# Kernel tuning notes

Hardware: AMD Instinct MI355X
Metric: run time of the kernel (lower is better)

## Reference

```python
import jax, jax.numpy as jnp
import numpy as np

HARD_DIST_CUTOFF = 2.0  # init kwarg of ExternalNeighbors


def setup_inputs() -> dict:
    key = jax.random.key(0)
    ks = jax.random.split(key, 6)
    n_mol, n_atoms = 128, 1024
    n_real = n_mol * n_atoms          # 131072
    n_pairs = 8388608                 # ~64 neighbors per atom
    coordinates = jax.random.normal(ks[0], (n_mol, n_atoms, 3), dtype=jnp.float32)
    real_atoms = jax.random.randint(ks[1], (n_real,), 0, n_mol * n_atoms, dtype=jnp.int64)
    shifts = jax.random.randint(ks[2], (n_pairs, 3), 0, 2, dtype=jnp.int32)
    cell = jax.random.normal(ks[3], (3, 3), dtype=jnp.float32)
    pair_first = jax.random.randint(ks[4], (n_pairs,), 0, n_real, dtype=jnp.int64)
    pair_second = jax.random.randint(ks[5], (n_pairs,), 0, n_real, dtype=jnp.int64)
    return {"coordinates": coordinates, "real_atoms": real_atoms, "shifts": shifts,
            "cell": cell, "pair_first": pair_first, "pair_second": pair_second}


def reference(coordinates, real_atoms, shifts, cell, pair_first, pair_second):
    n_mol, n_atoms, _ = coordinates.shape
    # gather real-atom coordinates from flattened (mol*atom, 3)
    atom_coordinates = coordinates.reshape(n_mol * n_atoms, 3)[real_atoms]
    # pair displacement with periodic shift: [n_pairs, 3]
    paircoord = (atom_coordinates[pair_second] - atom_coordinates[pair_first]
                 + shifts.astype(cell.dtype) @ cell)
    distflat = jnp.linalg.norm(paircoord, axis=1)  # [n_pairs]
    # torch version does boolean compaction (dynamic shape); in jax we keep
    # fixed shape and zero/mask-out pairs beyond the cutoff, returning the mask.
    mask = distflat < HARD_DIST_CUTOFF
    distflat_m = jnp.where(mask, distflat, 0.0)
    pair_first_m = jnp.where(mask, pair_first, -1)
    pair_second_m = jnp.where(mask, pair_second, -1)
    paircoord_m = jnp.where(mask[:, None], paircoord, 0.0)
    return distflat_m, pair_first_m, pair_second_m, paircoord_m, mask
```

## Files before the change

### kernel.cpp

```cpp
#include <hip/hip_runtime.h>


typedef float f32x4 __attribute__((ext_vector_type(4)));
typedef int   i32x4 __attribute__((ext_vector_type(4)));

#define HARD_DIST_CUTOFF 2.0f

__global__ __launch_bounds__(256) void build_gather_table(
    const float* __restrict__ coords,
    const int*   __restrict__ real_atoms,
    f32x4* __restrict__ tab,
    int n_real)
{
    const int i = blockIdx.x * blockDim.x + threadIdx.x;
    if (i < n_real) {
        const int a = __builtin_nontemporal_load(real_atoms + i);
        const float* c = coords + 3 * (size_t)a;
        f32x4 v;
        v.x = c[0]; v.y = c[1]; v.z = c[2]; v.w = 0.0f;
        tab[i] = v;
    }
}

__global__ __launch_bounds__(256, 8) void external_neighbors_v4(
    const f32x4* __restrict__ tab,
    const int*   __restrict__ shifts,
    const float* __restrict__ cell,
    const int*   __restrict__ pair_first,
    const int*   __restrict__ pair_second,
    float* __restrict__ out,
    int n_pairs)
{
    const float c00 = cell[0], c01 = cell[1], c02 = cell[2];
    const float c10 = cell[3], c11 = cell[4], c12 = cell[5];
    const float c20 = cell[6], c21 = cell[7], c22 = cell[8];

    const size_t N = (size_t)n_pairs;
    float* __restrict__ out_dist = out;
    float* __restrict__ out_pf   = out + N;
    float* __restrict__ out_ps   = out + 2 * N;
    float* __restrict__ out_pc   = out + 3 * N;
    float* __restrict__ out_mask = out + 6 * N;

    const int tid    = blockIdx.x * blockDim.x + threadIdx.x;
    const int nthr   = gridDim.x * blockDim.x;
    const int nbatch = n_pairs >> 2;

    for (int b = tid; b < nbatch; b += nthr) {
        const int base = b << 2;

        const i32x4 pf4 = __builtin_nontemporal_load(
            reinterpret_cast<const i32x4*>(pair_first + base));
        const i32x4 ps4 = __builtin_nontemporal_load(
            reinterpret_cast<const i32x4*>(pair_second + base));
        const i32x4* sh = reinterpret_cast<const i32x4*>(shifts + 3 * (size_t)base);
        const i32x4 sA = __builtin_nontemporal_load(sh + 0);
        const i32x4 sB = __builtin_nontemporal_load(sh + 1);
        const i32x4 sC = __builtin_nontemporal_load(sh + 2);

        const int pf[4] = {pf4.x, pf4.y, pf4.z, pf4.w};
        const int ps[4] = {ps4.x, ps4.y, ps4.z, ps4.w};
        const int s0[4] = {sA.x, sA.w, sB.z, sC.y};
        const int s1[4] = {sA.y, sB.x, sB.w, sC.z};
        const int s2[4] = {sA.z, sB.y, sC.x, sC.w};

        f32x4 A[4], B[4];
        #pragma unroll
        for (int k = 0; k < 4; ++k) A[k] = tab[pf[k]];
        #pragma unroll
        for (int k = 0; k < 4; ++k) B[k] = tab[ps[k]];

        f32x4 dist, pfo, pso, msk;
        float dxv[4], dyv[4], dzv[4];
        #pragma unroll
        for (int k = 0; k < 4; ++k) {
            const float f0 = (float)s0[k], f1 = (float)s1[k], f2 = (float)s2[k];
            const float dx = B[k].x - A[k].x + f0 * c00 + f1 * c10 + f2 * c20;
            const float dy = B[k].y - A[k].y + f0 * c01 + f1 * c11 + f2 * c21;
            const float dz = B[k].z - A[k].z + f0 * c02 + f1 * c12 + f2 * c22;
            const float d  = sqrtf(dx * dx + dy * dy + dz * dz);
            const bool  m  = d < HARD_DIST_CUTOFF;
            dist[k] = m ? d : 0.0f;
            pfo[k]  = m ? (float)pf[k] : -1.0f;
            pso[k]  = m ? (float)ps[k] : -1.0f;
            msk[k]  = m ? 1.0f : 0.0f;
            dxv[k]  = m ? dx : 0.0f;
            dyv[k]  = m ? dy : 0.0f;
            dzv[k]  = m ? dz : 0.0f;
        }

        __builtin_nontemporal_store(dist, reinterpret_cast<f32x4*>(out_dist + base));
        __builtin_nontemporal_store(pfo,  reinterpret_cast<f32x4*>(out_pf   + base));
        __builtin_nontemporal_store(pso,  reinterpret_cast<f32x4*>(out_ps   + base));
        __builtin_nontemporal_store(msk,  reinterpret_cast<f32x4*>(out_mask + base));
        f32x4* pc = reinterpret_cast<f32x4*>(out_pc + 3 * (size_t)base);
        const f32x4 p0 = {dxv[0], dyv[0], dzv[0], dxv[1]};
        const f32x4 p1 = {dyv[1], dzv[1], dxv[2], dyv[2]};
        const f32x4 p2 = {dzv[2], dxv[3], dyv[3], dzv[3]};
        __builtin_nontemporal_store(p0, pc + 0);
        __builtin_nontemporal_store(p1, pc + 1);
        __builtin_nontemporal_store(p2, pc + 2);
    }

    for (int p = (nbatch << 2) + tid; p < n_pairs; p += nthr) {
        const int pfs = pair_first[p];
        const int pss = pair_second[p];
        const float f0 = (float)shifts[3 * p + 0];
        const float f1 = (float)shifts[3 * p + 1];
        const float f2 = (float)shifts[3 * p + 2];
        const f32x4 Aa = tab[pfs];
        const f32x4 Bb = tab[pss];
        const float dx = Bb.x - Aa.x + f0 * c00 + f1 * c10 + f2 * c20;
        const float dy = Bb.y - Aa.y + f0 * c01 + f1 * c11 + f2 * c21;
        const float dz = Bb.z - Aa.z + f0 * c02 + f1 * c12 + f2 * c22;
        const float d  = sqrtf(dx * dx + dy * dy + dz * dz);
        const bool  m  = d < HARD_DIST_CUTOFF;
        out_dist[p] = m ? d : 0.0f;
        out_pf[p]   = m ? (float)pfs : -1.0f;
        out_ps[p]   = m ? (float)pss : -1.0f;
        out_pc[3*(size_t)p+0] = m ? dx : 0.0f;
        out_pc[3*(size_t)p+1] = m ? dy : 0.0f;
        out_pc[3*(size_t)p+2] = m ? dz : 0.0f;
        out_mask[p] = m ? 1.0f : 0.0f;
    }
}

__global__ __launch_bounds__(256) void external_neighbors_v2(
    const float* __restrict__ coords,
    const int*   __restrict__ real_atoms,
    const int*   __restrict__ shifts,
    const float* __restrict__ cell,
    const int*   __restrict__ pair_first,
    const int*   __restrict__ pair_second,
    float* __restrict__ out,
    int n_pairs)
{
    const float c00 = cell[0], c01 = cell[1], c02 = cell[2];
    const float c10 = cell[3], c11 = cell[4], c12 = cell[5];
    const float c20 = cell[6], c21 = cell[7], c22 = cell[8];
    const size_t N = (size_t)n_pairs;
    float* out_dist = out;
    float* out_pf   = out + N;
    float* out_ps   = out + 2 * N;
    float* out_pc   = out + 3 * N;
    float* out_mask = out + 6 * N;
    const int tid = blockIdx.x * blockDim.x + threadIdx.x;
    const int stride = gridDim.x * blockDim.x;
    for (int p = tid; p < n_pairs; p += stride) {
        const int pfs = pair_first[p];
        const int pss = pair_second[p];
        const float f0 = (float)shifts[3 * p + 0];
        const float f1 = (float)shifts[3 * p + 1];
        const float f2 = (float)shifts[3 * p + 2];
        const int iaa = real_atoms[pfs];
        const int ibb = real_atoms[pss];
        const float dx = coords[3*ibb+0] - coords[3*iaa+0] + f0*c00 + f1*c10 + f2*c20;
        const float dy = coords[3*ibb+1] - coords[3*iaa+1] + f0*c01 + f1*c11 + f2*c21;
        const float dz = coords[3*ibb+2] - coords[3*iaa+2] + f0*c02 + f1*c12 + f2*c22;
        const float d  = sqrtf(dx*dx + dy*dy + dz*dz);
        const bool  m  = d < HARD_DIST_CUTOFF;
        out_dist[p] = m ? d : 0.0f;
        out_pf[p]   = m ? (float)pfs : -1.0f;
        out_ps[p]   = m ? (float)pss : -1.0f;
        out_pc[3*(size_t)p+0] = m ? dx : 0.0f;
        out_pc[3*(size_t)p+1] = m ? dy : 0.0f;
        out_pc[3*(size_t)p+2] = m ? dz : 0.0f;
        out_mask[p] = m ? 1.0f : 0.0f;
    }
}

extern "C" void kernel_launch(void* const* d_in, const int* in_sizes, int n_in,
                              void* d_out, int out_size, void* d_ws, size_t ws_size,
                              hipStream_t stream) {
    const float* coords      = (const float*)d_in[0];
    const int*   real_atoms  = (const int*)d_in[1];
    const int*   shifts      = (const int*)d_in[2];
    const float* cell        = (const float*)d_in[3];
    const int*   pair_first  = (const int*)d_in[4];
    const int*   pair_second = (const int*)d_in[5];
    float*       out         = (float*)d_out;

    const int n_real  = in_sizes[1];
    const int n_pairs = in_sizes[4];

    const size_t tab_bytes = (size_t)n_real * sizeof(f32x4);

    if (ws_size >= tab_bytes) {
        f32x4* tab = (f32x4*)d_ws;
        build_gather_table<<<(n_real + 255) / 256, 256, 0, stream>>>(
            coords, real_atoms, tab, n_real);

        external_neighbors_v4<<<2048, 256, 0, stream>>>(
            tab, shifts, cell, pair_first, pair_second, out, n_pairs);
    } else {
        external_neighbors_v2<<<2048, 256, 0, stream>>>(
            coords, real_atoms, shifts, cell, pair_first, pair_second, out, n_pairs);
    }
}
```

Measured before the change: 442.8 us.

## Stage paircoord writes through LDS and launch one 4-pair batch per thread

Replaces the grid-stride loop with a non-persistent grid where each thread handles exactly four pairs, sized as n_pairs/1024 blocks. The interleaved paircoord output is transposed through LDS so each wave writes contiguous 16-byte chunks across lanes, aiming for fully coalesced stores instead of per-thread 48-byte strided writes. Input loads drop the nontemporal hint and the occupancy launch bound is removed. The fast path now requires n_pairs divisible by 1024 and adds a block-wide barrier plus 12 KB of LDS per block.

After: 404.8 us. 1.09x faster.

```diff
diff --git a/kernel.cpp b/kernel.cpp
--- a/kernel.cpp
+++ b/kernel.cpp
@@ -14,7 +14,7 @@
 {
     const int i = blockIdx.x * blockDim.x + threadIdx.x;
     if (i < n_real) {
-        const int a = __builtin_nontemporal_load(real_atoms + i);
+        const int a = real_atoms[i];
         const float* c = coords + 3 * (size_t)a;
         f32x4 v;
         v.x = c[0]; v.y = c[1]; v.z = c[2]; v.w = 0.0f;
@@ -22,7 +22,7 @@
     }
 }
 
-__global__ __launch_bounds__(256, 8) void external_neighbors_v4(
+__global__ __launch_bounds__(256) void external_neighbors_v6(
     const f32x4* __restrict__ tab,
     const int*   __restrict__ shifts,
     const float* __restrict__ cell,
@@ -31,6 +31,8 @@
     float* __restrict__ out,
     int n_pairs)
 {
+    __shared__ float lds_pc[4][768];
+
     const float c00 = cell[0], c01 = cell[1], c02 = cell[2];
     const float c10 = cell[3], c11 = cell[4], c12 = cell[5];
     const float c20 = cell[6], c21 = cell[7], c22 = cell[8];
@@ -42,86 +44,63 @@
     float* __restrict__ out_pc   = out + 3 * N;
     float* __restrict__ out_mask = out + 6 * N;
 
-    const int tid    = blockIdx.x * blockDim.x + threadIdx.x;
-    const int nthr   = gridDim.x * blockDim.x;
-    const int nbatch = n_pairs >> 2;
+    const int tid  = blockIdx.x * blockDim.x + threadIdx.x;
+    const int base = tid << 2;
+    const int wv   = threadIdx.x >> 6;
+    const int lane = threadIdx.x & 63;
 
-    for (int b = tid; b < nbatch; b += nthr) {
-        const int base = b << 2;
+    const i32x4 pf4 = *reinterpret_cast<const i32x4*>(pair_first  + base);
+    const i32x4 ps4 = *reinterpret_cast<const i32x4*>(pair_second + base);
+    const i32x4* sh = reinterpret_cast<const i32x4*>(shifts + 3 * (size_t)base);
+    const i32x4 sA = sh[0], sB = sh[1], sC = sh[2];
 
-        const i32x4 pf4 = __builtin_nontemporal_load(
-            reinterpret_cast<const i32x4*>(pair_first + base));
-        const i32x4 ps4 = __builtin_nontemporal_load(
-            reinterpret_cast<const i32x4*>(pair_second + base));
-        const i32x4* sh = reinterpret_cast<const i32x4*>(shifts + 3 * (size_t)base);
-        const i32x4 sA = __builtin_nontemporal_load(sh + 0);
-        const i32x4 sB = __builtin_nontemporal_load(sh + 1);
-        const i32x4 sC = __builtin_nontemporal_load(sh + 2);
+    const int pf[4] = {pf4.x, pf4.y, pf4.z, pf4.w};
+    const int ps[4] = {ps4.x, ps4.y, ps4.z, ps4.w};
+    const int s0[4] = {sA.x, sA.w, sB.z, sC.y};
+    const int s1[4] = {sA.y, sB.x, sB.w, sC.z};
+    const int s2[4] = {sA.z, sB.y, sC.x, sC.w};
 
-        const int pf[4] = {pf4.x, pf4.y, pf4.z, pf4.w};
-        const int ps[4] = {ps4.x, ps4.y, ps4.z, ps4.w};
-        const int s0[4] = {sA.x, sA.w, sB.z, sC.y};
-        const int s1[4] = {sA.y, sB.x, sB.w, sC.z};
-        const int s2[4] = {sA.z, sB.y, sC.x, sC.w};
+    f32x4 A[4], B[4];
+    #pragma unroll
+    for (int k = 0; k < 4; ++k) A[k] = tab[pf[k]];
+    #pragma unroll
+    for (int k = 0; k < 4; ++k) B[k] = tab[ps[k]];
 
-        f32x4 A[4], B[4];
-        #pragma unroll
-        for (int k = 0; k < 4; ++k) A[k] = tab[pf[k]];
-        #pragma unroll
-        for (int k = 0; k < 4; ++k) B[k] = tab[ps[k]];
-
-        f32x4 dist, pfo, pso, msk;
-        float dxv[4], dyv[4], dzv[4];
-        #pragma unroll
-        for (int k = 0; k < 4; ++k) {
-            const float f0 = (float)s0[k], f1 = (float)s1[k], f2 = (float)s2[k];
-            const float dx = B[k].x - A[k].x + f0 * c00 + f1 * c10 + f2 * c20;
-            const float dy = B[k].y - A[k].y + f0 * c01 + f1 * c11 + f2 * c21;
-            const float dz = B[k].z - A[k].z + f0 * c02 + f1 * c12 + f2 * c22;
-            const float d  = sqrtf(dx * dx + dy * dy + dz * dz);
-            const bool  m  = d < HARD_DIST_CUTOFF;
-            dist[k] = m ? d : 0.0f;
-            pfo[k]  = m ? (float)pf[k] : -1.0f;
-            pso[k]  = m ? (float)ps[k] : -1.0f;
-            msk[k]  = m ? 1.0f : 0.0f;
-            dxv[k]  = m ? dx : 0.0f;
-            dyv[k]  = m ? dy : 0.0f;
-            dzv[k]  = m ? dz : 0.0f;
-        }
-
-        __builtin_nontemporal_store(dist, reinterpret_cast<f32x4*>(out_dist + base));
-        __builtin_nontemporal_store(pfo,  reinterpret_cast<f32x4*>(out_pf   + base));
-        __builtin_nontemporal_store(pso,  reinterpret_cast<f32x4*>(out_ps   + base));
-        __builtin_nontemporal_store(msk,  reinterpret_cast<f32x4*>(out_mask + base));
-        f32x4* pc = reinterpret_cast<f32x4*>(out_pc + 3 * (size_t)base);
-        const f32x4 p0 = {dxv[0], dyv[0], dzv[0], dxv[1]};
-        const f32x4 p1 = {dyv[1], dzv[1], dxv[2], dyv[2]};
-        const f32x4 p2 = {dzv[2], dxv[3], dyv[3], dzv[3]};
-        __builtin_nontemporal_store(p0, pc + 0);
-        __builtin_nontemporal_store(p1, pc + 1);
-        __builtin_nontemporal_store(p2, pc + 2);
+    f32x4 dist, pfo, pso, msk;
+    float dxv[4], dyv[4], dzv[4];
+    #pragma unroll
+    for (int k = 0; k < 4; ++k) {
+        const float f0 = (float)s0[k], f1 = (float)s1[k], f2 = (float)s2[k];
+        const float dx = B[k].x - A[k].x + f0 * c00 + f1 * c10 + f2 * c20;
+        const float dy = B[k].y - A[k].y + f0 * c01 + f1 * c11 + f2 * c21;
+        const float dz = B[k].z - A[k].z + f0 * c02 + f1 * c12 + f2 * c22;
+        const float d  = sqrtf(dx * dx + dy * dy + dz * dz);
+        const bool  m  = d < HARD_DIST_CUTOFF;
+        dist[k] = m ? d : 0.0f;
+        pfo[k]  = m ? (float)pf[k] : -1.0f;
+        pso[k]  = m ? (float)ps[k] : -1.0f;
+        msk[k]  = m ? 1.0f : 0.0f;
+        dxv[k]  = m ? dx : 0.0f;
+        dyv[k]  = m ? dy : 0.0f;
+        dzv[k]  = m ? dz : 0.0f;
     }
 
-    for (int p = (nbatch << 2) + tid; p < n_pairs; p += nthr) {
-        const int pfs = pair_first[p];
-        const int pss = pair_second[p];
-        const float f0 = (float)shifts[3 * p + 0];
-        const float f1 = (float)shifts[3 * p + 1];
-        const float f2 = (float)shifts[3 * p + 2];
-        const f32x4 Aa = tab[pfs];
-        const f32x4 Bb = tab[pss];
-        const float dx = Bb.x - Aa.x + f0 * c00 + f1 * c10 + f2 * c20;
-        const float dy = Bb.y - Aa.y + f0 * c01 + f1 * c11 + f2 * c21;
-        const float dz = Bb.z - Aa.z + f0 * c02 + f1 * c12 + f2 * c22;
-        const float d  = sqrtf(dx * dx + dy * dy + dz * dz);
-        const bool  m  = d < HARD_DIST_CUTOFF;
-        out_dist[p] = m ? d : 0.0f;
-        out_pf[p]   = m ? (float)pfs : -1.0f;
-        out_ps[p]   = m ? (float)pss : -1.0f;
-        out_pc[3*(size_t)p+0] = m ? dx : 0.0f;
-        out_pc[3*(size_t)p+1] = m ? dy : 0.0f;
-        out_pc[3*(size_t)p+2] = m ? dz : 0.0f;
-        out_mask[p] = m ? 1.0f : 0.0f;
+    f32x4* myl = reinterpret_cast<f32x4*>(&lds_pc[wv][12 * lane]);
+    myl[0] = (f32x4){dxv[0], dyv[0], dzv[0], dxv[1]};
+    myl[1] = (f32x4){dyv[1], dzv[1], dxv[2], dyv[2]};
+    myl[2] = (f32x4){dzv[2], dxv[3], dyv[3], dzv[3]};
+    __syncthreads();
+
+    __builtin_nontemporal_store(dist, reinterpret_cast<f32x4*>(out_dist + base));
+    __builtin_nontemporal_store(pfo,  reinterpret_cast<f32x4*>(out_pf   + base));
+    __builtin_nontemporal_store(pso,  reinterpret_cast<f32x4*>(out_ps   + base));
+    __builtin_nontemporal_store(msk,  reinterpret_cast<f32x4*>(out_mask + base));
+
+    float* pcw = out_pc + 768 * (size_t)((blockIdx.x << 2) + wv);
+    #pragma unroll
+    for (int h = 0; h < 3; ++h) {
+        const f32x4 v = *reinterpret_cast<const f32x4*>(&lds_pc[wv][256 * h + 4 * lane]);
+        __builtin_nontemporal_store(v, reinterpret_cast<f32x4*>(pcw + 256 * h + 4 * lane));
     }
 }
 
@@ -185,12 +164,13 @@
 
     const size_t tab_bytes = (size_t)n_real * sizeof(f32x4);
 
-    if (ws_size >= tab_bytes) {
+    if (ws_size >= tab_bytes && (n_pairs % 1024) == 0) {
         f32x4* tab = (f32x4*)d_ws;
         build_gather_table<<<(n_real + 255) / 256, 256, 0, stream>>>(
             coords, real_atoms, tab, n_real);
 
-        external_neighbors_v4<<<2048, 256, 0, stream>>>(
+        const int grid = n_pairs / 1024;
+        external_neighbors_v6<<<grid, 256, 0, stream>>>(
             tab, shifts, cell, pair_first, pair_second, out, n_pairs);
     } else {
         external_neighbors_v2<<<2048, 256, 0, stream>>>(
```
